# Performance work log

Measured on AMD Instinct MI355X. Metric: run time of the kernel, lower is better.

The kernel has to match this reference:

```python
import jax, jax.numpy as jnp
import numpy as np

N, S, D = 2, 2048, 512
HEADS, HEAD_DIM = 8, 64
SCALE_BASE = 512.0
EPS = 1e-08


def xpos_apply(x, positions, downscale):
    # x: (B, S, d)  positions: (B, S) float
    d = x.shape[-1]
    half = jnp.arange(0, d, 2, dtype=jnp.float32)
    scale_vec = (half + 0.4 * d) / (1.4 * d)                      # (d/2,)
    power = positions[..., None] / SCALE_BASE                     # (B, S, 1)
    scale = scale_vec ** power                                    # (B, S, d/2)
    inv_freq = 1.0 / (10000.0 ** (half / d))                      # (d/2,)
    sinusoid = positions[..., None] * inv_freq                    # (B, S, d/2)
    sin = jnp.sin(sinusoid)
    cos = jnp.cos(sinusoid)
    if downscale:
        scale = 1.0 / scale
    # duplicate-interleave to full dim
    sin = jnp.repeat(sin, 2, axis=-1)
    cos = jnp.repeat(cos, 2, axis=-1)
    scale = jnp.repeat(scale, 2, axis=-1)
    x1 = x[..., 0::2]
    x2 = x[..., 1::2]
    rot = jnp.stack([-x2, x1], axis=-1).reshape(x.shape)          # rotate_every_two
    return (x * cos + rot * sin) * scale


def split_heads(x):
    # (N, S, H*Hd) -> (N*H, S, Hd)
    return x.reshape(N, S, HEADS, HEAD_DIM).transpose(0, 2, 1, 3).reshape(N * HEADS, S, HEAD_DIM)


def setup_inputs() -> dict:
    key = jax.random.key(0)
    ks = jax.random.split(key, 8)
    g = 1.0 / np.sqrt(D)
    return {
        'sequence': jax.random.normal(ks[0], (N, S, D), dtype=jnp.float32),
        'input_mask': jnp.ones((N, S), dtype=jnp.float32),
        'positions': jnp.tile(jnp.arange(S, dtype=jnp.int32), (N, 1)),
        'layer_num': 0,
        'Wq': jax.random.normal(ks[1], (D, D), dtype=jnp.float32) * g,
        'bq': jnp.zeros((D,), dtype=jnp.float32),
        'Wk': jax.random.normal(ks[2], (D, D), dtype=jnp.float32) * g,
        'bk': jnp.zeros((D,), dtype=jnp.float32),
        'Wv': jax.random.normal(ks[3], (D, D), dtype=jnp.float32) * g,
        'bv': jnp.zeros((D,), dtype=jnp.float32),
        'Wo': jax.random.normal(ks[4], (D, D), dtype=jnp.float32) * g,
        'bo': jnp.zeros((D,), dtype=jnp.float32),
    }


def reference(sequence, input_mask, positions, layer_num, Wq, bq, Wk, bk, Wv, bv, Wo, bo):
    scaling = HEAD_DIM ** (-0.5)
    posf = positions.astype(jnp.float32)

    Q = split_heads(sequence @ Wq.T + bq) * scaling               # (N*H, S, Hd)
    K = split_heads(sequence @ Wk.T + bk)
    V = split_heads(sequence @ Wv.T + bv)

    pos_h = jnp.repeat(posf, HEADS, axis=0)                       # 'n s -> (n h) s'
    K = xpos_apply(K, pos_h, downscale=True)
    Q = xpos_apply(Q, pos_h, downscale=False)

    A = jnp.einsum('nsd,ntd->nst', Q, K).reshape(N, HEADS, S, S)  # (N, H, S, S2)
    Vh = V.reshape(N, HEADS, S, HEAD_DIM)

    # causal mask: input_mask over kv dim, lower-triangular
    tri = jnp.tril(jnp.ones((S, S), dtype=jnp.float32))
    attn_mask = input_mask[:, None, None, :] * tri[None, None]    # (N, 1, S, S2)

    A = jax.nn.sigmoid(A) * attn_mask

    # stick-breaking decay: reverse-cumprod of (1 - A) along kv dim, shifted
    Af = jnp.flip(A, axis=(2, 3))
    C = jnp.exp(jnp.cumsum(jnp.log(1.0 - Af + EPS), axis=-1))
    C = jnp.flip(C, axis=(2, 3))
    C = jnp.concatenate([jnp.ones((N, HEADS, S, 1), dtype=C.dtype), C[..., :-1]], axis=-1)

    A = C * A
    attended = jnp.einsum('nhst,nhtd->nhsd', A, Vh)               # (N, H, S, Hd)
    attended = attended.transpose(0, 2, 1, 3).reshape(N, S, HEADS * HEAD_DIM)
    out = attended @ Wo.T + bo
    return out
```

## Files before the change

kernel.cpp:

```cpp
#include <hip/hip_runtime.h>
#include <math.h>

#define S_LEN 2048
#define DMODEL 512
#define HDIM 64
#define EPS_G 1e-8f

typedef __bf16 bf16x8 __attribute__((ext_vector_type(8)));
typedef __bf16 bf16x4 __attribute__((ext_vector_type(4)));
typedef float f32x4 __attribute__((ext_vector_type(4)));

__global__ __launch_bounds__(256) void cvt_kernel(
    const float* __restrict__ X, const float* __restrict__ Wq,
    const float* __restrict__ Wk, const float* __restrict__ Wv,
    const float* __restrict__ Wo,
    __bf16* __restrict__ Xb, __bf16* __restrict__ Wb, __bf16* __restrict__ Wob) {
  const int u = blockIdx.x * 256 + threadIdx.x;
  const float* src; __bf16* dst; int off;
  if (u < 524288)      { src = X;  dst = Xb;          off = u; }
  else if (u < 589824) { src = Wq; dst = Wb;          off = u - 524288; }
  else if (u < 655360) { src = Wk; dst = Wb + 262144; off = u - 589824; }
  else if (u < 720896) { src = Wv; dst = Wb + 524288; off = u - 655360; }
  else                 { src = Wo; dst = Wob;         off = u - 720896; }
  const float4 v = *(const float4*)(src + (size_t)off * 4);
  bf16x4 o;
  o[0] = (__bf16)v.x; o[1] = (__bf16)v.y; o[2] = (__bf16)v.z; o[3] = (__bf16)v.w;
  *(bf16x4*)(dst + (size_t)off * 4) = o;
}

__global__ __launch_bounds__(256, 2) void qkv_gemm(
    const __bf16* __restrict__ Xb, const __bf16* __restrict__ Wb,
    const float* __restrict__ bq, const float* __restrict__ bk, const float* __restrict__ bv,
    const int* __restrict__ pos,
    __bf16* __restrict__ Qh, __bf16* __restrict__ Kh, __bf16* __restrict__ Vt) {
  const int i0 = blockIdx.x << 6;
  const int h  = blockIdx.y;
  const int j0 = h << 6;

  __shared__ __bf16 Xs[64][72];
  __shared__ __bf16 Wls[3][64][72];

  const int tid = threadIdx.x;
  const int wv = tid >> 6, lane = tid & 63;
  const int l = lane & 15, seg = lane >> 4;
  const int sr = tid >> 2, sc = (tid & 3) << 4;

  f32x4 O[3][4];
#pragma unroll
  for (int w = 0; w < 3; ++w)
#pragma unroll
    for (int r4 = 0; r4 < 4; ++r4) O[w][r4] = (f32x4){0.f, 0.f, 0.f, 0.f};

  bf16x8 xr0, xr1, wr[3][2];
#define LOADQKV(K0)                                                                   \
  {                                                                                   \
    const __bf16* xp = Xb + (size_t)(i0 + sr) * 512 + (K0) + sc;                      \
    xr0 = *(const bf16x8*)xp; xr1 = *(const bf16x8*)(xp + 8);                         \
    _Pragma("unroll")                                                                 \
    for (int w = 0; w < 3; ++w) {                                                     \
      const __bf16* wp = Wb + (size_t)w * 262144 + (size_t)(j0 + sr) * 512 + (K0) + sc;\
      wr[w][0] = *(const bf16x8*)wp; wr[w][1] = *(const bf16x8*)(wp + 8);             \
    }                                                                                 \
  }

  LOADQKV(0)
  for (int k0 = 0; k0 < 512; k0 += 64) {
    __syncthreads();
    *(bf16x8*)&Xs[sr][sc]     = xr0;
    *(bf16x8*)&Xs[sr][sc + 8] = xr1;
#pragma unroll
    for (int w = 0; w < 3; ++w) {
      *(bf16x8*)&Wls[w][sr][sc]     = wr[w][0];
      *(bf16x8*)&Wls[w][sr][sc + 8] = wr[w][1];
    }
    __syncthreads();
    if (k0 < 448) LOADQKV(k0 + 64)

    bf16x8 a0[4], a1[4];
#pragma unroll
    for (int r4 = 0; r4 < 4; ++r4) {
      a0[r4] = *(const bf16x8*)&Xs[r4 * 16 + l][seg * 8];
      a1[r4] = *(const bf16x8*)&Xs[r4 * 16 + l][seg * 8 + 32];
    }
#pragma unroll
    for (int w = 0; w < 3; ++w) {
      bf16x8 b0 = *(const bf16x8*)&Wls[w][wv * 16 + l][seg * 8];
      bf16x8 b1 = *(const bf16x8*)&Wls[w][wv * 16 + l][seg * 8 + 32];
#pragma unroll
      for (int r4 = 0; r4 < 4; ++r4) {
        O[w][r4] = __builtin_amdgcn_mfma_f32_16x16x32_bf16(a0[r4], b0, O[w][r4], 0, 0, 0);
        O[w][r4] = __builtin_amdgcn_mfma_f32_16x16x32_bf16(a1[r4], b1, O[w][r4], 0, 0, 0);
      }
    }
  }

  const int d = wv * 16 + l;
  const float bbq = bq[j0 + d], bbk = bk[j0 + d], bbv = bv[j0 + d];
#pragma unroll
  for (int r4 = 0; r4 < 4; ++r4)
#pragma unroll
    for (int reg = 0; reg < 4; ++reg) {
      O[0][r4][reg] += bbq; O[1][r4][reg] += bbk; O[2][r4][reg] += bbv;
    }

  const int n = i0 >> 11, sb = i0 & 2047;
  const int nh = (n << 3) + h;

  const float kp   = (float)(d >> 1);
  const float invf = exp2f(-0.41524100f * kp) * 0.15915494f;
  const float l2sv = log2f((2.f * kp + 25.6f) * (1.f / 89.6f));
  float pv_[4][4];
#pragma unroll
  for (int r4 = 0; r4 < 4; ++r4)
#pragma unroll
    for (int reg = 0; reg < 4; ++reg)
      pv_[r4][reg] = (float)pos[n * S_LEN + sb + r4 * 16 + (seg << 2) + reg];

  __syncthreads();

#pragma unroll
  for (int r4 = 0; r4 < 4; ++r4)
#pragma unroll
    for (int reg = 0; reg < 4; ++reg) {
      const int row = r4 * 16 + (seg << 2) + reg;
      const float p = pv_[r4][reg];
      const float rev0 = p * invf;
      const float rev  = rev0 - floorf(rev0);
      const float sn = __builtin_amdgcn_sinf(rev);
      const float cn = __builtin_amdgcn_cosf(rev);
      const float sq = exp2f(p * (1.f / 512.f) * l2sv);
      const float sQ = sq * 0.125f;
      const float sK = __builtin_amdgcn_rcpf(sq);
      float x  = O[0][r4][reg];
      float xp = __shfl_xor(x, 1);
      Xs[row][d] = (__bf16)((((d & 1) ? (x * cn + xp * sn) : (x * cn - xp * sn))) * sQ);
      x  = O[1][r4][reg];
      xp = __shfl_xor(x, 1);
      Wls[0][row][d] = (__bf16)((((d & 1) ? (x * cn + xp * sn) : (x * cn - xp * sn))) * sK);
      Wls[1][row][d] = (__bf16)O[2][r4][reg];
    }
  __syncthreads();

  __bf16* qdst = Qh + (((size_t)nh * S_LEN + sb + sr) << 6) + sc;
  *(bf16x8*)qdst       = *(bf16x8*)&Xs[sr][sc];
  *(bf16x8*)(qdst + 8) = *(bf16x8*)&Xs[sr][sc + 8];
  __bf16* kdst = Kh + (((size_t)nh * S_LEN + sb + sr) << 6) + sc;
  *(bf16x8*)kdst       = *(bf16x8*)&Wls[0][sr][sc];
  *(bf16x8*)(kdst + 8) = *(bf16x8*)&Wls[0][sr][sc + 8];

  const int dv = tid >> 2, part = tid & 3;
  __bf16 tmp[16];
#pragma unroll
  for (int i = 0; i < 16; ++i) tmp[i] = Wls[1][part * 16 + i][dv];
  __bf16* vdst = Vt + (((size_t)(nh * 64 + dv)) << 11) + sb + part * 16;
  *(bf16x8*)vdst       = *(bf16x8*)&tmp[0];
  *(bf16x8*)(vdst + 8) = *(bf16x8*)&tmp[8];
}

__global__ __launch_bounds__(256, 2) void attn_chunk(
    const __bf16* __restrict__ Qh, const __bf16* __restrict__ Kh,
    const __bf16* __restrict__ Vt, const float* __restrict__ imask,
    __bf16* __restrict__ att, float* __restrict__ PartO,
    float* __restrict__ PartP, float* __restrict__ PartA0) {
  const int id = 1279 - (int)blockIdx.x;
  const int nh = id & 15;
  const int t  = id >> 4;
  int rb, c, nc;
  if (t < 8)       { rb = t; c = 0; nc = 1; }
  else if (t < 24) { int u = t - 8;  rb = 8  + (u >> 1); c = u & 1;     nc = 2; }
  else if (t < 48) { int u = t - 24; rb = 16 + u / 3;    c = u - 3 * (u / 3); nc = 3; }
  else             { int u = t - 48; rb = 24 + (u >> 2); c = u & 3;     nc = 4; }
  const int T   = rb + 1;
  const int bsz = T / nc;
  const int rem = T - bsz * nc;
  const int szc  = bsz + ((c < rem) ? 1 : 0);
  const int skip = c * bsz + ((c < rem) ? c : rem);
  const int hi = rb - skip;
  const int lo = hi - szc + 1;

  const int n = nh >> 3, h = nh & 7;
  const int tid = threadIdx.x;
  const int wv = tid >> 6, lane = tid & 63;
  const int l = lane & 15, seg = lane >> 4;
  const int sg4 = seg << 2;
  const int pr = tid >> 3, pc = (tid & 7) << 3;

  __shared__ __bf16 Ks16[64][72];
  __shared__ __bf16 Vt16[64][72];
  __shared__ __bf16 cs16[64][72];
  __shared__ float msk[64];
  __shared__ float v0buf[64];

  const __bf16* qbase =
      Qh + (((size_t)nh * S_LEN + rb * 64 + wv * 16 + l) << 6);
  const bf16x8 aq0 = *(const bf16x8*)(qbase + seg * 8);
  const bf16x8 aq1 = *(const bf16x8*)(qbase + seg * 8 + 32);

  f32x4 O[4];
  f32x4 pend[4];
  float Crow = 1.f;
  float a0k0 = 0.f;
#pragma unroll
  for (int d_ = 0; d_ < 4; ++d_) {
    O[d_] = (f32x4){0.f, 0.f, 0.f, 0.f};
    pend[d_] = (f32x4){0.f, 0.f, 0.f, 0.f};
  }

  bf16x8 kp0, kp1, vp0, vp1;
  float mp = 0.f;
#define LOADKV(JT)                                                                     \
  kp0 = *(const bf16x8*)(Kh + (((size_t)nh * S_LEN + (JT) * 64 + pr) << 6) + pc);      \
  kp1 = *(const bf16x8*)(Kh + (((size_t)nh * S_LEN + (JT) * 64 + 32 + pr) << 6) + pc); \
  vp0 = *(const bf16x8*)(Vt + (((size_t)(nh * 64 + pr)) << 11) + (JT) * 64 + pc);      \
  vp1 = *(const bf16x8*)(Vt + (((size_t)(nh * 64 + 32 + pr)) << 11) + (JT) * 64 + pc); \
  if (tid < 64) mp = imask[n * S_LEN + (JT) * 64 + tid];

  LOADKV(hi)

  for (int jt = hi; jt >= lo; --jt) {
    __syncthreads();
    *(bf16x8*)&Ks16[pr][pc]      = kp0;
    *(bf16x8*)&Ks16[32 + pr][pc] = kp1;
    *(bf16x8*)&Vt16[pr][pc]      = vp0;
    *(bf16x8*)&Vt16[32 + pr][pc] = vp1;
    if (tid < 64) msk[tid] = mp;
    if ((tid & 7) == 0) {
      v0buf[pr]      = (float)vp0[0];
      v0buf[32 + pr] = (float)vp1[0];
    }
    __syncthreads();
    if (jt > lo) { LOADKV(jt - 1) }

    f32x4 Sv[4];
    __builtin_amdgcn_s_setprio(1);
#pragma unroll
    for (int nt = 0; nt < 4; ++nt) {
      bf16x8 bk0 = *(const bf16x8*)&Ks16[nt * 16 + l][seg * 8];
      bf16x8 bk1 = *(const bf16x8*)&Ks16[nt * 16 + l][seg * 8 + 32];
      f32x4 z = (f32x4){0.f, 0.f, 0.f, 0.f};
      z = __builtin_amdgcn_mfma_f32_16x16x32_bf16(bk0, aq0, z, 0, 0, 0);
      z = __builtin_amdgcn_mfma_f32_16x16x32_bf16(bk1, aq1, z, 0, 0, 0);
      Sv[nt] = z;
    }
    __builtin_amdgcn_s_setprio(0);

    const bool diag = (jt == rb);
    const int qoff = wv * 16 + l;

    float a_[4][4];
#pragma unroll
    for (int nt = 0; nt < 4; ++nt) {
      const float4 m4 = *(const float4*)&msk[nt * 16 + sg4];
      a_[nt][0] = m4.x * __builtin_amdgcn_rcpf(1.f + __expf(-Sv[nt][0]));
      a_[nt][1] = m4.y * __builtin_amdgcn_rcpf(1.f + __expf(-Sv[nt][1]));
      a_[nt][2] = m4.z * __builtin_amdgcn_rcpf(1.f + __expf(-Sv[nt][2]));
      a_[nt][3] = m4.w * __builtin_amdgcn_rcpf(1.f + __expf(-Sv[nt][3]));
    }
    if (diag) {
#pragma unroll
      for (int nt = 0; nt < 4; ++nt)
#pragma unroll
        for (int reg = 0; reg < 4; ++reg)
          if (nt * 16 + sg4 + reg > qoff) a_[nt][reg] = 0.f;
    }

    float t_[4][4], gp[4], f3s[4];
#pragma unroll
    for (int nt = 0; nt < 4; ++nt) {
      const float f0 = 1.f - a_[nt][0] + EPS_G;
      const float f1 = 1.f - a_[nt][1] + EPS_G;
      const float f2 = 1.f - a_[nt][2] + EPS_G;
      const float f3 = 1.f - a_[nt][3] + EPS_G;
      t_[nt][3] = f3;
      t_[nt][2] = f2 * f3;
      t_[nt][1] = f1 * t_[nt][2];
      t_[nt][0] = f0 * t_[nt][1];
      gp[nt] = t_[nt][0];
      f3s[nt] = f3;
    }

    float S_[4], GP[4], Xs_[4], Yb[4];
#pragma unroll
    for (int nt = 0; nt < 4; ++nt) {
      const float b = __shfl_xor(gp[nt], 16);
      const float cc = __shfl_xor(gp[nt], 32);
      const float dd = __shfl_xor(b, 32);
      const float cd = cc * dd;
      const float low  = (seg & 1) ? cd : b * cd;
      const float high = (seg & 1) ? 1.f : b;
      S_[nt] = (seg & 2) ? high : low;
      GP[nt] = gp[nt] * b * cd;
      Xs_[nt] = __shfl_up(f3s[nt], 16);
      Yb[nt] = __shfl(f3s[nt], 48 + l);
    }
    const float T2 = GP[3], T1 = T2 * GP[2], T0 = T1 * GP[1];
    const float Tarr[4] = {T0, T1, T2, 1.f};
    const float Ptile = T0 * GP[0];
    const float A0 = __shfl(a_[0][0], l);

#pragma unroll
    for (int nt = 0; nt < 4; ++nt) {
      const float wc = S_[nt] * Tarr[nt] * Crow;
      float cv0 = a_[nt][0] * Xs_[nt] * gp[nt] * wc;
      const float cv0s0 = (nt == 0)
          ? ((jt == 0 && nc == 1) ? a_[0][0] : 0.f)
          : a_[nt][0] * Yb[nt - 1] * Tarr[nt - 1] * Crow;
      if (seg == 0) cv0 = cv0s0;
      const float cv1 = a_[nt][1] * t_[nt][0] * wc;
      const float cv2 = a_[nt][2] * t_[nt][1] * wc;
      const float cv3 = a_[nt][3] * t_[nt][2] * wc;
      bf16x4 pk;
      pk[0] = (__bf16)cv0; pk[1] = (__bf16)cv1;
      pk[2] = (__bf16)cv2; pk[3] = (__bf16)cv3;
      *(bf16x4*)&cs16[wv * 16 + l][nt * 16 + sg4] = pk;
    }

    const float f63 = Yb[3];
    const float s0 = A0 * Ptile * Crow;
    Crow *= Ptile;
    if (jt == 0) a0k0 = A0;
#pragma unroll
    for (int dblk = 0; dblk < 4; ++dblk) {
      O[dblk][0] += pend[dblk][0] * f63;
      O[dblk][1] += pend[dblk][1] * f63;
      O[dblk][2] += pend[dblk][2] * f63;
      O[dblk][3] += pend[dblk][3] * f63;
      const float4 v4 = *(const float4*)&v0buf[dblk * 16 + sg4];
      pend[dblk][0] = s0 * v4.x; pend[dblk][1] = s0 * v4.y;
      pend[dblk][2] = s0 * v4.z; pend[dblk][3] = s0 * v4.w;
    }

    bf16x8 bc0 = *(const bf16x8*)&cs16[wv * 16 + l][seg * 8];
    bf16x8 bc1 = *(const bf16x8*)&cs16[wv * 16 + l][seg * 8 + 32];
    __builtin_amdgcn_s_setprio(1);
#pragma unroll
    for (int dblk = 0; dblk < 4; ++dblk) {
      bf16x8 av0 = *(const bf16x8*)&Vt16[dblk * 16 + l][seg * 8];
      bf16x8 av1 = *(const bf16x8*)&Vt16[dblk * 16 + l][seg * 8 + 32];
      O[dblk] = __builtin_amdgcn_mfma_f32_16x16x32_bf16(av0, bc0, O[dblk], 0, 0, 0);
      O[dblk] = __builtin_amdgcn_mfma_f32_16x16x32_bf16(av1, bc1, O[dblk], 0, 0, 0);
    }
    __builtin_amdgcn_s_setprio(0);
  }

  if (lo > 0) {
    const int m = lo << 6;
    const float mb = imask[n * S_LEN + m - 1];
    const __bf16* kb = Kh + (((size_t)nh * S_LEN + m - 1) << 6) + seg * 16;
    bf16x8 kb0 = *(const bf16x8*)kb, kb1 = *(const bf16x8*)(kb + 8);
    bf16x8 q0 = *(const bf16x8*)(qbase + seg * 16);
    bf16x8 q1 = *(const bf16x8*)(qbase + seg * 16 + 8);
    float sc_ = 0.f;
#pragma unroll
    for (int j = 0; j < 8; ++j)
      sc_ += (float)q0[j] * (float)kb0[j] + (float)q1[j] * (float)kb1[j];
    sc_ += __shfl_xor(sc_, 16);
    sc_ += __shfl_xor(sc_, 32);
    const float fbl = 1.f - mb * __builtin_amdgcn_rcpf(1.f + __expf(-sc_)) + EPS_G;
#pragma unroll
    for (int dblk = 0; dblk < 4; ++dblk) {
      O[dblk][0] += pend[dblk][0] * fbl;
      O[dblk][1] += pend[dblk][1] * fbl;
      O[dblk][2] += pend[dblk][2] * fbl;
      O[dblk][3] += pend[dblk][3] * fbl;
    }
  }

  if (nc == 1) {
    __bf16* arow = att + ((size_t)(n * S_LEN + rb * 64 + wv * 16 + l)) * DMODEL + h * HDIM;
#pragma unroll
    for (int dblk = 0; dblk < 4; ++dblk) {
      bf16x4 ob;
      ob[0] = (__bf16)O[dblk][0]; ob[1] = (__bf16)O[dblk][1];
      ob[2] = (__bf16)O[dblk][2]; ob[3] = (__bf16)O[dblk][3];
      *(bf16x4*)(arow + dblk * 16 + sg4) = ob;
    }
  } else {
    const int slot = nh * 72 + (t - 8);
    float* po = PartO + (size_t)slot * 4096 + (wv * 16 + l) * 64;
#pragma unroll
    for (int dblk = 0; dblk < 4; ++dblk) {
      float4 v;
      v.x = O[dblk][0]; v.y = O[dblk][1]; v.z = O[dblk][2]; v.w = O[dblk][3];
      *(float4*)(po + dblk * 16 + sg4) = v;
    }
    if (seg == 0) {
      PartP[slot * 64 + wv * 16 + l] = Crow;
      if (lo == 0)
        PartA0[(nh * 24 + rb - 8) * 64 + wv * 16 + l] = a0k0;
    }
  }
}

__global__ __launch_bounds__(256) void combine_kernel(
    const float* __restrict__ PartO, const float* __restrict__ PartP,
    const float* __restrict__ PartA0, const __bf16* __restrict__ Vt,
    __bf16* __restrict__ att) {
  const int b = blockIdx.x;
  const int nh = b / 24;
  const int rb = 8 + (b - nh * 24);
  const int nc = (rb < 16) ? 2 : ((rb < 24) ? 3 : 4);
  const int t0 = (rb < 16) ? 8 + ((rb - 8) << 1)
               : (rb < 24) ? 24 + (rb - 16) * 3
                           : 48 + ((rb - 24) << 2);
  const int n = nh >> 3, h = nh & 7;
  const int tid = threadIdx.x;
  const int r = tid >> 2, db = (tid & 3) << 4;

  float acc[16];
#pragma unroll
  for (int j = 0; j < 16; ++j) acc[j] = 0.f;
  float fac = 1.f;
  for (int c = 0; c < nc; ++c) {
    const int slot = nh * 72 + (t0 - 8) + c;
    const float* po = PartO + (size_t)slot * 4096 + r * 64 + db;
    const float P = PartP[slot * 64 + r];
#pragma unroll
    for (int q = 0; q < 4; ++q) {
      const float4 v = *(const float4*)(po + q * 4);
      acc[q * 4 + 0] += fac * v.x; acc[q * 4 + 1] += fac * v.y;
      acc[q * 4 + 2] += fac * v.z; acc[q * 4 + 3] += fac * v.w;
    }
    fac *= P;
  }
  const float a0 = PartA0[(nh * 24 + rb - 8) * 64 + r];
#pragma unroll
  for (int j = 0; j < 16; ++j)
    acc[j] += a0 * (float)Vt[(((size_t)(nh * 64 + db + j)) << 11)];

  __bf16 ob[16];
#pragma unroll
  for (int j = 0; j < 16; ++j) ob[j] = (__bf16)acc[j];
  __bf16* dst = att + ((size_t)(n * S_LEN + rb * 64 + r)) * DMODEL + h * HDIM + db;
  *(bf16x8*)dst       = *(bf16x8*)&ob[0];
  *(bf16x8*)(dst + 8) = *(bf16x8*)&ob[8];
}

__global__ __launch_bounds__(256, 2) void out_gemm(const __bf16* __restrict__ Xa,
                                                   const __bf16* __restrict__ Wob,
                                                   const float* __restrict__ bo,
                                                   float* __restrict__ Out) {
  const int i0 = blockIdx.x << 6, j0 = blockIdx.y << 7;
  __shared__ __bf16 As[64][72];
  __shared__ __bf16 Bs[128][72];

  const int tid = threadIdx.x;
  const int wv = tid >> 6, lane = tid & 63;
  const int l = lane & 15, seg = lane >> 4;
  const int sr = tid >> 2, sc = (tid & 3) << 4;

  f32x4 O[2][4];
#pragma unroll
  for (int j = 0; j < 2; ++j)
#pragma unroll
    for (int r4 = 0; r4 < 4; ++r4) O[j][r4] = (f32x4){0.f, 0.f, 0.f, 0.f};

  bf16x8 ar0, ar1, br[2][2];
#define LOADOUT(K0)                                                          \
  {                                                                          \
    const __bf16* xp = Xa + (size_t)(i0 + sr) * 512 + (K0) + sc;             \
    ar0 = *(const bf16x8*)xp; ar1 = *(const bf16x8*)(xp + 8);                \
    _Pragma("unroll")                                                        \
    for (int ps = 0; ps < 2; ++ps) {                                         \
      const __bf16* wp = Wob + (size_t)(j0 + ps * 64 + sr) * 512 + (K0) + sc;\
      br[ps][0] = *(const bf16x8*)wp; br[ps][1] = *(const bf16x8*)(wp + 8);  \
    }                                                                        \
  }

  LOADOUT(0)
  for (int k0 = 0; k0 < 512; k0 += 64) {
    __syncthreads();
    *(bf16x8*)&As[sr][sc]     = ar0;
    *(bf16x8*)&As[sr][sc + 8] = ar1;
#pragma unroll
    for (int ps = 0; ps < 2; ++ps) {
      *(bf16x8*)&Bs[ps * 64 + sr][sc]     = br[ps][0];
      *(bf16x8*)&Bs[ps * 64 + sr][sc + 8] = br[ps][1];
    }
    __syncthreads();
    if (k0 < 448) LOADOUT(k0 + 64)

    bf16x8 a0[4], a1[4];
#pragma unroll
    for (int r4 = 0; r4 < 4; ++r4) {
      a0[r4] = *(const bf16x8*)&As[r4 * 16 + l][seg * 8];
      a1[r4] = *(const bf16x8*)&As[r4 * 16 + l][seg * 8 + 32];
    }
#pragma unroll
    for (int j = 0; j < 2; ++j) {
      const int u = wv + 4 * j;
      bf16x8 b0 = *(const bf16x8*)&Bs[u * 16 + l][seg * 8];
      bf16x8 b1 = *(const bf16x8*)&Bs[u * 16 + l][seg * 8 + 32];
#pragma unroll
      for (int r4 = 0; r4 < 4; ++r4) {
        O[j][r4] = __builtin_amdgcn_mfma_f32_16x16x32_bf16(a0[r4], b0, O[j][r4], 0, 0, 0);
        O[j][r4] = __builtin_amdgcn_mfma_f32_16x16x32_bf16(a1[r4], b1, O[j][r4], 0, 0, 0);
      }
    }
  }

#pragma unroll
  for (int j = 0; j < 2; ++j) {
    const int u = wv + 4 * j;
    const float bb = bo[j0 + u * 16 + l];
#pragma unroll
    for (int r4 = 0; r4 < 4; ++r4)
#pragma unroll
      for (int reg = 0; reg < 4; ++reg) {
        const int m = r4 * 16 + (seg << 2) + reg;
        Out[(size_t)(i0 + m) * 512 + j0 + u * 16 + l] = O[j][r4][reg] + bb;
      }
  }
}

extern "C" void kernel_launch(void* const* d_in, const int* in_sizes, int n_in,
                              void* d_out, int out_size, void* d_ws, size_t ws_size,
                              hipStream_t stream) {
  (void)in_sizes; (void)n_in; (void)out_size; (void)ws_size;
  const float* seq  = (const float*)d_in[0];
  const float* mask = (const float*)d_in[1];
  const int*   pos  = (const int*)d_in[2];
  const float* Wq = (const float*)d_in[4];
  const float* bq = (const float*)d_in[5];
  const float* Wk = (const float*)d_in[6];
  const float* bk = (const float*)d_in[7];
  const float* Wv = (const float*)d_in[8];
  const float* bv = (const float*)d_in[9];
  const float* Wo = (const float*)d_in[10];
  const float* bo = (const float*)d_in[11];
  float* out = (float*)d_out;

  char* base = (char*)d_ws;
  __bf16* att = (__bf16*)base;
  __bf16* Qh  = (__bf16*)(base + ( 4u << 20));
  __bf16* Kh  = (__bf16*)(base + ( 8u << 20));
  __bf16* Vt  = (__bf16*)(base + (12u << 20));
  __bf16* Wb  = (__bf16*)(base + (16u << 20));
  __bf16* Wob = (__bf16*)(base + (18u << 20));
  __bf16* Xb  = (__bf16*)(base + (19u << 20));
  float* PartO  = (float*)(base + (23u << 20));
  float* PartP  = (float*)(base + (42u << 20));
  float* PartA0 = (float*)(base + (43u << 20));

  cvt_kernel<<<3072, 256, 0, stream>>>(seq, Wq, Wk, Wv, Wo, Xb, Wb, Wob);
  qkv_gemm<<<dim3(64, 8), 256, 0, stream>>>(Xb, Wb, bq, bk, bv, pos, Qh, Kh, Vt);
  attn_chunk<<<1280, 256, 0, stream>>>(Qh, Kh, Vt, mask, att, PartO, PartP, PartA0);
  combine_kernel<<<384, 256, 0, stream>>>(PartO, PartP, PartA0, Vt, att);
  out_gemm<<<dim3(64, 4), 256, 0, stream>>>(att, Wob, bo, out);
}
```

Baseline: 148.9 us.

## Double-buffer K/V shared tiles to drop one barrier per iteration

Result: no change. 151.3 us (+1.7%).

```diff
diff --git a/kernel.cpp b/kernel.cpp
--- a/kernel.cpp
+++ b/kernel.cpp
@@ -185,11 +185,11 @@
   const int sg4 = seg << 2;
   const int pr = tid >> 3, pc = (tid & 7) << 3;
 
-  __shared__ __bf16 Ks16[64][72];
-  __shared__ __bf16 Vt16[64][72];
+  __shared__ __bf16 Ks16[2][64][72];
+  __shared__ __bf16 Vt16[2][64][72];
   __shared__ __bf16 cs16[64][72];
-  __shared__ float msk[64];
-  __shared__ float v0buf[64];
+  __shared__ float msk[2][64];
+  __shared__ float v0buf[2][64];
 
   const __bf16* qbase =
       Qh + (((size_t)nh * S_LEN + rb * 64 + wv * 16 + l) << 6);
@@ -206,37 +206,42 @@
     pend[d_] = (f32x4){0.f, 0.f, 0.f, 0.f};
   }
 
+  const __bf16* kptr = Kh + (((size_t)nh * S_LEN + hi * 64 + pr) << 6) + pc;
+  const __bf16* vptr = Vt + (((size_t)(nh * 64 + pr)) << 11) + hi * 64 + pc;
+  const float*  mptr = imask + n * S_LEN + hi * 64 + tid;
+
   bf16x8 kp0, kp1, vp0, vp1;
   float mp = 0.f;
-#define LOADKV(JT)                                                                     \
-  kp0 = *(const bf16x8*)(Kh + (((size_t)nh * S_LEN + (JT) * 64 + pr) << 6) + pc);      \
-  kp1 = *(const bf16x8*)(Kh + (((size_t)nh * S_LEN + (JT) * 64 + 32 + pr) << 6) + pc); \
-  vp0 = *(const bf16x8*)(Vt + (((size_t)(nh * 64 + pr)) << 11) + (JT) * 64 + pc);      \
-  vp1 = *(const bf16x8*)(Vt + (((size_t)(nh * 64 + 32 + pr)) << 11) + (JT) * 64 + pc); \
-  if (tid < 64) mp = imask[n * S_LEN + (JT) * 64 + tid];
-
-  LOADKV(hi)
-
+#define LOADKV_P()                                              \
+  kp0 = *(const bf16x8*)kptr;                                   \
+  kp1 = *(const bf16x8*)(kptr + (32 << 6));                     \
+  vp0 = *(const bf16x8*)vptr;                                   \
+  vp1 = *(const bf16x8*)(vptr + ((size_t)32 << 11));            \
+  if (tid < 64) mp = *mptr;                                     \
+  kptr -= (64 << 6); vptr -= 64; mptr -= 64;
+
+  LOADKV_P()
+  *(bf16x8*)&Ks16[0][pr][pc]      = kp0;
+  *(bf16x8*)&Ks16[0][32 + pr][pc] = kp1;
+  *(bf16x8*)&Vt16[0][pr][pc]      = vp0;
+  *(bf16x8*)&Vt16[0][32 + pr][pc] = vp1;
+  if (tid < 64) msk[0][tid] = mp;
+  if ((tid & 7) == 0) {
+    v0buf[0][pr]      = (float)vp0[0];
+    v0buf[0][32 + pr] = (float)vp1[0];
+  }
+  __syncthreads();
+
+  int cur = 0;
   for (int jt = hi; jt >= lo; --jt) {
-    __syncthreads();
-    *(bf16x8*)&Ks16[pr][pc]      = kp0;
-    *(bf16x8*)&Ks16[32 + pr][pc] = kp1;
-    *(bf16x8*)&Vt16[pr][pc]      = vp0;
-    *(bf16x8*)&Vt16[32 + pr][pc] = vp1;
-    if (tid < 64) msk[tid] = mp;
-    if ((tid & 7) == 0) {
-      v0buf[pr]      = (float)vp0[0];
-      v0buf[32 + pr] = (float)vp1[0];
-    }
-    __syncthreads();
-    if (jt > lo) { LOADKV(jt - 1) }
+    if (jt > lo) { LOADKV_P() }
 
     f32x4 Sv[4];
     __builtin_amdgcn_s_setprio(1);
 #pragma unroll
     for (int nt = 0; nt < 4; ++nt) {
-      bf16x8 bk0 = *(const bf16x8*)&Ks16[nt * 16 + l][seg * 8];
-      bf16x8 bk1 = *(const bf16x8*)&Ks16[nt * 16 + l][seg * 8 + 32];
+      bf16x8 bk0 = *(const bf16x8*)&Ks16[cur][nt * 16 + l][seg * 8];
+      bf16x8 bk1 = *(const bf16x8*)&Ks16[cur][nt * 16 + l][seg * 8 + 32];
       f32x4 z = (f32x4){0.f, 0.f, 0.f, 0.f};
       z = __builtin_amdgcn_mfma_f32_16x16x32_bf16(bk0, aq0, z, 0, 0, 0);
       z = __builtin_amdgcn_mfma_f32_16x16x32_bf16(bk1, aq1, z, 0, 0, 0);
@@ -250,7 +255,7 @@
     float a_[4][4];
 #pragma unroll
     for (int nt = 0; nt < 4; ++nt) {
-      const float4 m4 = *(const float4*)&msk[nt * 16 + sg4];
+      const float4 m4 = *(const float4*)&msk[cur][nt * 16 + sg4];
       a_[nt][0] = m4.x * __builtin_amdgcn_rcpf(1.f + __expf(-Sv[nt][0]));
       a_[nt][1] = m4.y * __builtin_amdgcn_rcpf(1.f + __expf(-Sv[nt][1]));
       a_[nt][2] = m4.z * __builtin_amdgcn_rcpf(1.f + __expf(-Sv[nt][2]));
@@ -325,7 +330,7 @@
       O[dblk][1] += pend[dblk][1] * f63;
       O[dblk][2] += pend[dblk][2] * f63;
       O[dblk][3] += pend[dblk][3] * f63;
-      const float4 v4 = *(const float4*)&v0buf[dblk * 16 + sg4];
+      const float4 v4 = *(const float4*)&v0buf[cur][dblk * 16 + sg4];
       pend[dblk][0] = s0 * v4.x; pend[dblk][1] = s0 * v4.y;
       pend[dblk][2] = s0 * v4.z; pend[dblk][3] = s0 * v4.w;
     }
@@ -335,12 +340,27 @@
     __builtin_amdgcn_s_setprio(1);
 #pragma unroll
     for (int dblk = 0; dblk < 4; ++dblk) {
-      bf16x8 av0 = *(const bf16x8*)&Vt16[dblk * 16 + l][seg * 8];
-      bf16x8 av1 = *(const bf16x8*)&Vt16[dblk * 16 + l][seg * 8 + 32];
+      bf16x8 av0 = *(const bf16x8*)&Vt16[cur][dblk * 16 + l][seg * 8];
+      bf16x8 av1 = *(const bf16x8*)&Vt16[cur][dblk * 16 + l][seg * 8 + 32];
       O[dblk] = __builtin_amdgcn_mfma_f32_16x16x32_bf16(av0, bc0, O[dblk], 0, 0, 0);
       O[dblk] = __builtin_amdgcn_mfma_f32_16x16x32_bf16(av1, bc1, O[dblk], 0, 0, 0);
     }
     __builtin_amdgcn_s_setprio(0);
+
+    if (jt > lo) {
+      const int nxt = cur ^ 1;
+      *(bf16x8*)&Ks16[nxt][pr][pc]      = kp0;
+      *(bf16x8*)&Ks16[nxt][32 + pr][pc] = kp1;
+      *(bf16x8*)&Vt16[nxt][pr][pc]      = vp0;
+      *(bf16x8*)&Vt16[nxt][32 + pr][pc] = vp1;
+      if (tid < 64) msk[nxt][tid] = mp;
+      if ((tid & 7) == 0) {
+        v0buf[nxt][pr]      = (float)vp0[0];
+        v0buf[nxt][32 + pr] = (float)vp1[0];
+      }
+      __syncthreads();
+      cur = nxt;
+    }
   }
 
   if (lo > 0) {
```

## Process two KV tiles per barrier pair with double-buffered shared memory

Applied to the files above, without the earlier changes.

New measurement: 154.3 us. 1.04x slower.

```diff
diff --git a/kernel.cpp b/kernel.cpp
--- a/kernel.cpp
+++ b/kernel.cpp
@@ -185,11 +185,11 @@
   const int sg4 = seg << 2;
   const int pr = tid >> 3, pc = (tid & 7) << 3;
 
-  __shared__ __bf16 Ks16[64][72];
-  __shared__ __bf16 Vt16[64][72];
-  __shared__ __bf16 cs16[64][72];
-  __shared__ float msk[64];
-  __shared__ float v0buf[64];
+  __shared__ __bf16 Ks16[2][64][72];
+  __shared__ __bf16 Vt16[2][64][72];
+  __shared__ __bf16 cs16[2][64][72];
+  __shared__ float msk[2][64];
+  __shared__ float v0buf[2][64];
 
   const __bf16* qbase =
       Qh + (((size_t)nh * S_LEN + rb * 64 + wv * 16 + l) << 6);
@@ -206,37 +206,33 @@
     pend[d_] = (f32x4){0.f, 0.f, 0.f, 0.f};
   }
 
-  bf16x8 kp0, kp1, vp0, vp1;
-  float mp = 0.f;
-#define LOADKV(JT)                                                                     \
-  kp0 = *(const bf16x8*)(Kh + (((size_t)nh * S_LEN + (JT) * 64 + pr) << 6) + pc);      \
-  kp1 = *(const bf16x8*)(Kh + (((size_t)nh * S_LEN + (JT) * 64 + 32 + pr) << 6) + pc); \
-  vp0 = *(const bf16x8*)(Vt + (((size_t)(nh * 64 + pr)) << 11) + (JT) * 64 + pc);      \
-  vp1 = *(const bf16x8*)(Vt + (((size_t)(nh * 64 + 32 + pr)) << 11) + (JT) * 64 + pc); \
-  if (tid < 64) mp = imask[n * S_LEN + (JT) * 64 + tid];
-
-  LOADKV(hi)
-
-  for (int jt = hi; jt >= lo; --jt) {
-    __syncthreads();
-    *(bf16x8*)&Ks16[pr][pc]      = kp0;
-    *(bf16x8*)&Ks16[32 + pr][pc] = kp1;
-    *(bf16x8*)&Vt16[pr][pc]      = vp0;
-    *(bf16x8*)&Vt16[32 + pr][pc] = vp1;
-    if (tid < 64) msk[tid] = mp;
-    if ((tid & 7) == 0) {
-      v0buf[pr]      = (float)vp0[0];
-      v0buf[32 + pr] = (float)vp1[0];
-    }
-    __syncthreads();
-    if (jt > lo) { LOADKV(jt - 1) }
-
+  bf16x8 kp0[2], kp1[2], vp0[2], vp1[2];
+  float mp[2] = {0.f, 0.f};
+#define LOADKV(JT, B)                                                                      \
+  kp0[B] = *(const bf16x8*)(Kh + (((size_t)nh * S_LEN + (JT) * 64 + pr) << 6) + pc);       \
+  kp1[B] = *(const bf16x8*)(Kh + (((size_t)nh * S_LEN + (JT) * 64 + 32 + pr) << 6) + pc);  \
+  vp0[B] = *(const bf16x8*)(Vt + (((size_t)(nh * 64 + pr)) << 11) + (JT) * 64 + pc);       \
+  vp1[B] = *(const bf16x8*)(Vt + (((size_t)(nh * 64 + 32 + pr)) << 11) + (JT) * 64 + pc);  \
+  if (tid < 64) mp[B] = imask[n * S_LEN + (JT) * 64 + tid];
+
+#define STAGE(B)                                            \
+  *(bf16x8*)&Ks16[B][pr][pc]      = kp0[B];                 \
+  *(bf16x8*)&Ks16[B][32 + pr][pc] = kp1[B];                 \
+  *(bf16x8*)&Vt16[B][pr][pc]      = vp0[B];                 \
+  *(bf16x8*)&Vt16[B][32 + pr][pc] = vp1[B];                 \
+  if (tid < 64) msk[B][tid] = mp[B];                        \
+  if ((tid & 7) == 0) {                                     \
+    v0buf[B][pr]      = (float)vp0[B][0];                   \
+    v0buf[B][32 + pr] = (float)vp1[B][0];                   \
+  }
+
+  auto tile_body = [&](int jt, int B) {
     f32x4 Sv[4];
     __builtin_amdgcn_s_setprio(1);
 #pragma unroll
     for (int nt = 0; nt < 4; ++nt) {
-      bf16x8 bk0 = *(const bf16x8*)&Ks16[nt * 16 + l][seg * 8];
-      bf16x8 bk1 = *(const bf16x8*)&Ks16[nt * 16 + l][seg * 8 + 32];
+      bf16x8 bk0 = *(const bf16x8*)&Ks16[B][nt * 16 + l][seg * 8];
+      bf16x8 bk1 = *(const bf16x8*)&Ks16[B][nt * 16 + l][seg * 8 + 32];
       f32x4 z = (f32x4){0.f, 0.f, 0.f, 0.f};
       z = __builtin_amdgcn_mfma_f32_16x16x32_bf16(bk0, aq0, z, 0, 0, 0);
       z = __builtin_amdgcn_mfma_f32_16x16x32_bf16(bk1, aq1, z, 0, 0, 0);
@@ -250,7 +246,7 @@
     float a_[4][4];
 #pragma unroll
     for (int nt = 0; nt < 4; ++nt) {
-      const float4 m4 = *(const float4*)&msk[nt * 16 + sg4];
+      const float4 m4 = *(const float4*)&msk[B][nt * 16 + sg4];
       a_[nt][0] = m4.x * __builtin_amdgcn_rcpf(1.f + __expf(-Sv[nt][0]));
       a_[nt][1] = m4.y * __builtin_amdgcn_rcpf(1.f + __expf(-Sv[nt][1]));
       a_[nt][2] = m4.z * __builtin_amdgcn_rcpf(1.f + __expf(-Sv[nt][2]));
@@ -312,7 +308,7 @@
       bf16x4 pk;
       pk[0] = (__bf16)cv0; pk[1] = (__bf16)cv1;
       pk[2] = (__bf16)cv2; pk[3] = (__bf16)cv3;
-      *(bf16x4*)&cs16[wv * 16 + l][nt * 16 + sg4] = pk;
+      *(bf16x4*)&cs16[B][wv * 16 + l][nt * 16 + sg4] = pk;
     }
 
     const float f63 = Yb[3];
@@ -325,22 +321,39 @@
       O[dblk][1] += pend[dblk][1] * f63;
       O[dblk][2] += pend[dblk][2] * f63;
       O[dblk][3] += pend[dblk][3] * f63;
-      const float4 v4 = *(const float4*)&v0buf[dblk * 16 + sg4];
+      const float4 v4 = *(const float4*)&v0buf[B][dblk * 16 + sg4];
       pend[dblk][0] = s0 * v4.x; pend[dblk][1] = s0 * v4.y;
       pend[dblk][2] = s0 * v4.z; pend[dblk][3] = s0 * v4.w;
     }
 
-    bf16x8 bc0 = *(const bf16x8*)&cs16[wv * 16 + l][seg * 8];
-    bf16x8 bc1 = *(const bf16x8*)&cs16[wv * 16 + l][seg * 8 + 32];
+    bf16x8 bc0 = *(const bf16x8*)&cs16[B][wv * 16 + l][seg * 8];
+    bf16x8 bc1 = *(const bf16x8*)&cs16[B][wv * 16 + l][seg * 8 + 32];
     __builtin_amdgcn_s_setprio(1);
 #pragma unroll
     for (int dblk = 0; dblk < 4; ++dblk) {
-      bf16x8 av0 = *(const bf16x8*)&Vt16[dblk * 16 + l][seg * 8];
-      bf16x8 av1 = *(const bf16x8*)&Vt16[dblk * 16 + l][seg * 8 + 32];
+      bf16x8 av0 = *(const bf16x8*)&Vt16[B][dblk * 16 + l][seg * 8];
+      bf16x8 av1 = *(const bf16x8*)&Vt16[B][dblk * 16 + l][seg * 8 + 32];
       O[dblk] = __builtin_amdgcn_mfma_f32_16x16x32_bf16(av0, bc0, O[dblk], 0, 0, 0);
       O[dblk] = __builtin_amdgcn_mfma_f32_16x16x32_bf16(av1, bc1, O[dblk], 0, 0, 0);
     }
     __builtin_amdgcn_s_setprio(0);
+  };
+
+  LOADKV(hi, 0)
+  if (hi - 1 >= lo) { LOADKV(hi - 1, 1) }
+
+  for (int jt = hi; jt >= lo; jt -= 2) {
+    const bool two = (jt - 1 >= lo);
+    __syncthreads();
+    STAGE(0)
+    if (two) { STAGE(1) }
+    __syncthreads();
+    if (jt - 2 >= lo) {
+      LOADKV(jt - 2, 0)
+      if (jt - 3 >= lo) { LOADKV(jt - 3, 1) }
+    }
+    tile_body(jt, 0);
+    if (two) tile_body(jt - 1, 1);
   }
 
   if (lo > 0) {
```
